# Performance work log

Measured on AMD Instinct MI355X. Metric: run time of the kernel, lower is better.

The kernel has to match this reference:

```python
import jax, jax.numpy as jnp
import numpy as np

N, E, LE, C = 20000, 320000, 640000, 128
EPS = 1e-7  # GENConv message eps


def _ln(x, g, b):
    # torch.nn.LayerNorm, eps=1e-5
    m = jnp.mean(x, axis=-1, keepdims=True)
    v = jnp.var(x, axis=-1, keepdims=True)
    return (x - m) * jax.lax.rsqrt(v + 1e-5) * g + b


def _mlp(x, W1, b1, g, b, W2, b2):
    # GENConv MLP, num_layers=2, norm='layer': Linear -> LayerNorm -> ReLU -> Linear
    h = jax.nn.relu(_ln(x @ W1 + b1, g, b))
    return h @ W2 + b2


def _gen_deep(x, src, dst, edge_attr, num_nodes, p):
    # DeepGCNLayer 'res+': norm -> relu -> dropout(eval=identity) -> GENConv -> + x
    h = jax.nn.relu(_ln(x, p['pre_g'], p['pre_b']))
    # GENConv message: relu(x_j [+ edge_attr]) + eps
    msg = h[src]
    if edge_attr is not None:
        msg = msg + edge_attr
    msg = jax.nn.relu(msg) + EPS  # [E, C]
    # softmax aggregation per destination segment, per channel
    logits = msg * p['t']
    mx = jax.ops.segment_max(logits, dst, num_segments=num_nodes)
    alpha = jnp.exp(logits - mx[dst])
    denom = jax.ops.segment_sum(alpha, dst, num_segments=num_nodes)
    aggr = jax.ops.segment_sum(alpha * msg, dst, num_segments=num_nodes)
    aggr = aggr / jnp.where(denom == 0, 1.0, denom)
    out = aggr + h  # GENConv root skip: out + x_r
    out = _mlp(out, p['W1'], p['b1'], p['ln_g'], p['ln_b'], p['W2'], p['b2'])
    return x + out  # res+ residual


def setup_inputs() -> dict:
    key = jax.random.key(0)
    ks = iter(jax.random.split(key, 16))
    s = 0.05
    d = {}
    d['v_x'] = jax.random.normal(next(ks), (N, C), jnp.float32)
    d['e_x'] = jax.random.normal(next(ks), (E, C), jnp.float32)
    d['v_edge_index'] = jax.random.randint(next(ks), (2, E), 0, N)
    d['e_edge_index'] = jax.random.randint(next(ks), (2, LE), 0, E)
    for pfx in ('e_', 'n_'):
        d[pfx + 'pre_g'] = jnp.ones((C,), jnp.float32)
        d[pfx + 'pre_b'] = jnp.zeros((C,), jnp.float32)
        d[pfx + 't'] = jnp.array(1.0, jnp.float32)
        d[pfx + 'W1'] = jax.random.normal(next(ks), (C, 2 * C), jnp.float32) * s
        d[pfx + 'b1'] = jnp.zeros((2 * C,), jnp.float32)
        d[pfx + 'ln_g'] = jnp.ones((2 * C,), jnp.float32)
        d[pfx + 'ln_b'] = jnp.zeros((2 * C,), jnp.float32)
        d[pfx + 'W2'] = jax.random.normal(next(ks), (2 * C, C), jnp.float32) * s
        d[pfx + 'b2'] = jnp.zeros((C,), jnp.float32)
    return d


def reference(v_x, e_x, v_edge_index, e_edge_index,
              e_pre_g, e_pre_b, e_t, e_W1, e_b1, e_ln_g, e_ln_b, e_W2, e_b2,
              n_pre_g, n_pre_b, n_t, n_W1, n_b1, n_ln_g, n_ln_b, n_W2, n_b2):
    ep = dict(pre_g=e_pre_g, pre_b=e_pre_b, t=e_t, W1=e_W1, b1=e_b1,
              ln_g=e_ln_g, ln_b=e_ln_b, W2=e_W2, b2=e_b2)
    npar = dict(pre_g=n_pre_g, pre_b=n_pre_b, t=n_t, W1=n_W1, b1=n_b1,
                ln_g=n_ln_g, ln_b=n_ln_b, W2=n_W2, b2=n_b2)
    # edge layer: GENConv over the line graph (no edge_attr)
    e_out = _gen_deep(e_x, e_edge_index[0], e_edge_index[1], None, E, ep)
    # node layer: GENConv over node graph with updated edge features as edge_attr
    v_out = _gen_deep(v_x, v_edge_index[0], v_edge_index[1], e_out, N, npar)
    return (v_out, e_out)
```

## Files before the change

kernel.cpp:

```cpp
#include <hip/hip_runtime.h>
#include <hip/hip_bf16.h>

#define GEN_EPS 1e-7f

typedef __attribute__((ext_vector_type(8))) short short8;
typedef __attribute__((ext_vector_type(4))) float f32x4;

__global__ void prep_all(
    const float* __restrict__ eW1, const float* __restrict__ eW2,
    const float* __restrict__ nW1, const float* __restrict__ nW2,
    short* __restrict__ eW1P, short* __restrict__ eW2P, short* __restrict__ nW1P,
    short* __restrict__ nW2P,
    const int* __restrict__ e_dst, const int* __restrict__ v_dst,
    int* __restrict__ ce, int* __restrict__ cn, int LE, int En, int nCNT,
    const float* __restrict__ ex, const float* __restrict__ vx,
    const float* __restrict__ eg, const float* __restrict__ eb,
    const float* __restrict__ ng, const float* __restrict__ nb_,
    __hip_bfloat16* __restrict__ he, __hip_bfloat16* __restrict__ hn, int E, int N) {
  int b = blockIdx.x;
  int tid = threadIdx.x;

  if (b < 768) {
    const float* W;
    short* WP;
    int R, Cc, c;
    if (b < 256) {
      W = eW1; WP = eW1P; R = 128; Cc = 256; c = b;
    } else if (b < 384) {
      W = eW2; WP = eW2P; R = 256; Cc = 128; c = b - 256;
    } else if (b < 640) {
      W = nW1; WP = nW1P; R = 128; Cc = 256; c = b - 384;
    } else {
      W = nW2; WP = nW2P; R = 256; Cc = 128; c = b - 640;
    }
    size_t tbase = (size_t)(c >> 4) * (size_t)(16 * R);
    int rsub = c & 15;
    for (int k = tid; k < R; k += blockDim.x) {
      __hip_bfloat16 bv = __float2bfloat16(W[(size_t)k * Cc + c]);
      int kk = k & 31;
      WP[tbase + (size_t)(k >> 5) * 512 + (kk >> 3) * 128 + rsub * 8 + (kk & 7)] =
          *(short*)&bv;
    }
    return;
  }
  b -= 768;

  if (b < nCNT) {
    int i = b * 256 + tid;
    if (i < LE)
      atomicAdd(&ce[e_dst[i]], 1);
    else if (i < LE + En)
      atomicAdd(&cn[v_dst[i - LE]], 1);
    return;
  }
  b -= nCNT;

  int l32 = tid & 31;
  int rr = b * 8 + ((tid & 255) >> 5);
  const float* x;
  const float* g;
  const float* bb;
  __hip_bfloat16* h;
  int r;
  if (rr < E) {
    x = ex; g = eg; bb = eb; h = he; r = rr;
  } else if (rr < E + N) {
    x = vx; g = ng; bb = nb_; h = hn; r = rr - E;
  } else {
    return;
  }
  float4 v = ((const float4*)(x + (size_t)r * 128))[l32];
  float s = v.x + v.y + v.z + v.w;
#pragma unroll
  for (int o = 16; o; o >>= 1) s += __shfl_xor(s, o);
  float m = s * (1.0f / 128.0f);
  float d0 = v.x - m, d1 = v.y - m, d2 = v.z - m, d3 = v.w - m;
  float q = d0 * d0 + d1 * d1 + d2 * d2 + d3 * d3;
#pragma unroll
  for (int o = 16; o; o >>= 1) q += __shfl_xor(q, o);
  float rstd = rsqrtf(q * (1.0f / 128.0f) + 1e-5f);
  float4 gv = ((const float4*)g)[l32];
  float4 bv = ((const float4*)bb)[l32];
  float2 h01, h23;
  h01.x = fmaxf(fmaf(d0 * rstd, gv.x, bv.x), 0.0f);
  h01.y = fmaxf(fmaf(d1 * rstd, gv.y, bv.y), 0.0f);
  h23.x = fmaxf(fmaf(d2 * rstd, gv.z, bv.z), 0.0f);
  h23.y = fmaxf(fmaf(d3 * rstd, gv.w, bv.w), 0.0f);
  __hip_bfloat162 p0 = __float22bfloat162_rn(h01);
  __hip_bfloat162 p1 = __float22bfloat162_rn(h23);
  uint2 u;
  u.x = *(uint*)&p0;
  u.y = *(uint*)&p1;
  ((uint2*)(h + (size_t)r * 128))[l32] = u;
}

__global__ void scan_block_sums_all(const int* __restrict__ ce, const int* __restrict__ cn,
                                    int* __restrict__ bsums, int nbE, int E, int N) {
  __shared__ int sm[256];
  int b = blockIdx.x;
  const int* counts;
  int M, bb;
  int* bs;
  if (b < nbE) {
    counts = ce; M = E; bb = b; bs = bsums;
  } else {
    counts = cn; M = N; bb = b - nbE; bs = bsums + 512;
  }
  int t = threadIdx.x;
  int base = bb * 1024 + t * 4;
  int s = 0;
#pragma unroll
  for (int i = 0; i < 4; i++) {
    int idx = base + i;
    if (idx < M) s += counts[idx];
  }
  sm[t] = s;
  __syncthreads();
  for (int o = 128; o; o >>= 1) {
    if (t < o) sm[t] += sm[t + o];
    __syncthreads();
  }
  if (t == 0) bs[bb] = sm[0];
}

__global__ void scan_bsums_all(int* bsums, int nbE, int nbN) {
  __shared__ int sm[512];
  int* bs = bsums + blockIdx.x * 512;
  int nb = (blockIdx.x == 0) ? nbE : nbN;
  int t = threadIdx.x;
  int v = (t < nb) ? bs[t] : 0;
  sm[t] = v;
  __syncthreads();
  for (int o = 1; o < 512; o <<= 1) {
    int u = (t >= o) ? sm[t - o] : 0;
    __syncthreads();
    sm[t] += u;
    __syncthreads();
  }
  if (t < nb) bs[t] = sm[t] - v;
}

__global__ void scan_write_all(const int* __restrict__ ce, const int* __restrict__ cn,
                               const int* __restrict__ bsums, int* __restrict__ off_e,
                               int* __restrict__ off_n, int* __restrict__ cur_e,
                               int* __restrict__ cur_n, int nbE, int E, int N, int LE,
                               int En) {
  __shared__ int sm[256];
  int b = blockIdx.x;
  const int* counts;
  const int* bs;
  int* off;
  int* cursor;
  int M, nnz, bb;
  if (b < nbE) {
    counts = ce; M = E; nnz = LE; bb = b; bs = bsums; off = off_e; cursor = cur_e;
  } else {
    counts = cn; M = N; nnz = En; bb = b - nbE; bs = bsums + 512; off = off_n;
    cursor = cur_n;
  }
  int t = threadIdx.x;
  int base = bb * 1024 + t * 4;
  int c[4];
  int s = 0;
#pragma unroll
  for (int i = 0; i < 4; i++) {
    int idx = base + i;
    c[i] = (idx < M) ? counts[idx] : 0;
    s += c[i];
  }
  sm[t] = s;
  __syncthreads();
  for (int o = 1; o < 256; o <<= 1) {
    int v = (t >= o) ? sm[t - o] : 0;
    __syncthreads();
    sm[t] += v;
    __syncthreads();
  }
  int p = bs[bb] + sm[t] - s;
#pragma unroll
  for (int i = 0; i < 4; i++) {
    int idx = base + i;
    if (idx < M) {
      off[idx] = p;
      cursor[idx] = p;
      p += c[i];
    }
  }
  if (bb == 0 && t == 0) off[M] = nnz;
}

__global__ void fill_all(const int* __restrict__ e_src, const int* __restrict__ e_dst,
                         const int* __restrict__ v_src, const int* __restrict__ v_dst,
                         int* __restrict__ cur_e, int* __restrict__ cur_n,
                         int* __restrict__ csrs_e, int* __restrict__ csrs_n,
                         int* __restrict__ csre_n, int LE, int En) {
  int i = blockIdx.x * blockDim.x + threadIdx.x;
  if (i < LE) {
    int p = atomicAdd(&cur_e[e_dst[i]], 1);
    csrs_e[p] = e_src[i];
  } else if (i < LE + En) {
    int j = i - LE;
    int p = atomicAdd(&cur_n[v_dst[j]], 1);
    csrs_n[p] = v_src[j];
    csre_n[p] = j;
  }
}

template <bool HAS_EATTR>
__global__ __launch_bounds__(256) void aggregate_kernel(
    const __hip_bfloat16* __restrict__ h, const int* __restrict__ off,
    const int* __restrict__ csr_src, const int* __restrict__ csr_eid,
    const ushort* __restrict__ eattr, const float* __restrict__ tptr,
    uint* __restrict__ yP, int M) {
  int lane = threadIdx.x & 63;
  int r = blockIdx.x * 4 + (threadIdx.x >> 6);
  if (r >= M) return;
  const float t = tptr[0];
  float2 hv = __bfloat1622float2(((const __hip_bfloat162*)(h + (size_t)r * 128))[lane]);
  int e0 = off[r], e1 = off[r + 1];
  float d0 = 0.0f, d1 = 0.0f, a0 = 0.0f, a1 = 0.0f;
  for (int e = e0; e < e1; e += 4) {
    int n = e1 - e;
    float2 mv[4];
#pragma unroll
    for (int u = 0; u < 4; u++) {
      int ee = (u < n) ? e + u : e;
      int s = csr_src[ee];
      mv[u] = __bfloat1622float2(((const __hip_bfloat162*)(h + (size_t)s * 128))[lane]);
    }
    if (HAS_EATTR) {
#pragma unroll
      for (int u = 0; u < 4; u++) {
        int ee = (u < n) ? e + u : e;
        int id = csr_eid[ee];
        uint ea = ((const uint*)(eattr + (size_t)id * 128))[lane];
        float2 ef = __bfloat1622float2(*(__hip_bfloat162*)&ea);
        mv[u].x += ef.x;
        mv[u].y += ef.y;
      }
    }
#pragma unroll
    for (int u = 0; u < 4; u++) {
      float w = (u < n) ? 1.0f : 0.0f;
      float m0 = fmaxf(mv[u].x, 0.0f) + GEN_EPS;
      float m1 = fmaxf(mv[u].y, 0.0f) + GEN_EPS;
      float al0 = __expf(m0 * t) * w, al1 = __expf(m1 * t) * w;
      d0 += al0;
      d1 += al1;
      a0 = fmaf(al0, m0, a0);
      a1 = fmaf(al1, m1, a1);
    }
  }
  float2 yv;
  yv.x = (e1 > e0 ? a0 / d0 : 0.0f) + hv.x;
  yv.y = (e1 > e0 ? a1 / d1 : 0.0f) + hv.y;
  __hip_bfloat162 yb2 = __float22bfloat162_rn(yv);
  yP[(r >> 4) * 1024 + (lane >> 4) * 256 + (r & 15) * 16 + (lane & 15)] = *(uint*)&yb2;
}

template <bool WRITE_BF16>
__global__ __launch_bounds__(512, 2) void mlp_kernel(
    const float* __restrict__ x, const short* yP, const short* __restrict__ W1P,
    const float* __restrict__ b1, const float* __restrict__ lng,
    const float* __restrict__ lnb, const short* __restrict__ W2P,
    const float* __restrict__ b2, float* __restrict__ out, ushort* out16,
    int ntiles, int stride, int M) {
  __shared__ short W1s[128 * 256];
  __shared__ short W2s[256 * 128];
  __shared__ short scr[8][2][16 * 34];

  const int tid = threadIdx.x, lane = tid & 63, wv = tid >> 6;
  const int rA = lane & 15, hi = lane >> 4;
  const int kA = hi * 8, jrow = hi * 4;
  const int foW = lane * 8;
  const int foA = rA * 32 + kA;

  {
    const short8* g1 = (const short8*)W1P;
    short8* l1 = (short8*)W1s;
#pragma unroll
    for (int i = 0; i < 8; i++) l1[i * 512 + tid] = g1[i * 512 + tid];
    const short8* g2 = (const short8*)W2P;
    short8* l2 = (short8*)W2s;
#pragma unroll
    for (int i = 0; i < 8; i++) l2[i * 512 + tid] = g2[i * 512 + tid];
  }

  float b1v[16], lngv[16], lnbv[16], b2v[8];
#pragma unroll
  for (int ct = 0; ct < 16; ct++) {
    int col = ct * 16 + rA;
    b1v[ct] = b1[col];
    lngv[ct] = lng[col];
    lnbv[ct] = lnb[col];
  }
#pragma unroll
  for (int ct = 0; ct < 8; ct++) b2v[ct] = b2[ct * 16 + rA];

  __syncthreads();

  int t = blockIdx.x * 8 + wv;
  short8 yA0, yA1, yA2, yA3;
  if (t < ntiles) {
    const short* yb = yP + (size_t)t * 2048 + foA;
    yA0 = *(const short8*)(yb);
    yA1 = *(const short8*)(yb + 512);
    yA2 = *(const short8*)(yb + 1024);
    yA3 = *(const short8*)(yb + 1536);
  }

  for (; t < ntiles; t += stride) {
    const int row0 = t * 16;

    f32x4 C1[16];
#pragma unroll
    for (int i = 0; i < 16; i++) C1[i] = (f32x4)0.0f;
#pragma unroll
    for (int kc = 0; kc < 4; kc++) {
      short8 a = (kc == 0) ? yA0 : (kc == 1) ? yA1 : (kc == 2) ? yA2 : yA3;
#pragma unroll
      for (int ct = 0; ct < 16; ct++) {
        short8 B = *(const short8*)&W1s[(ct * 4 + kc) * 512 + foW];
        C1[ct] = __builtin_amdgcn_mfma_f32_16x16x32_bf16(a, B, C1[ct], 0, 0, 0);
      }
    }

    {
      int tn = t + stride;
      int tc = (tn < ntiles) ? tn : t;
      const short* yb = yP + (size_t)tc * 2048 + foA;
      yA0 = *(const short8*)(yb);
      yA1 = *(const short8*)(yb + 512);
      yA2 = *(const short8*)(yb + 1024);
      yA3 = *(const short8*)(yb + 1536);
    }

    float xv[32];
#pragma unroll
    for (int ct = 0; ct < 8; ct++)
#pragma unroll
      for (int j = 0; j < 4; j++) {
        int row = row0 + jrow + j;
        int rr = (row < M) ? row : (M - 1);
        xv[ct * 4 + j] = x[(size_t)rr * 128 + ct * 16 + rA];
      }

#pragma unroll
    for (int ct = 0; ct < 16; ct++)
#pragma unroll
      for (int j = 0; j < 4; j++) C1[ct][j] += b1v[ct];

    float mean[4], rstd[4];
#pragma unroll
    for (int j = 0; j < 4; j++) {
      float p = 0.0f, q = 0.0f;
#pragma unroll
      for (int ct = 0; ct < 16; ct++) {
        p += C1[ct][j];
        q = fmaf(C1[ct][j], C1[ct][j], q);
      }
#pragma unroll
      for (int o = 1; o < 16; o <<= 1) {
        p += __shfl_xor(p, o);
        q += __shfl_xor(q, o);
      }
      float m = p * (1.0f / 256.0f);
      mean[j] = m;
      rstd[j] = rsqrtf(q * (1.0f / 256.0f) - m * m + 1e-5f);
    }

    f32x4 C2[8];
#pragma unroll
    for (int i = 0; i < 8; i++) C2[i] = (f32x4)0.0f;
#pragma unroll
    for (int kc = 0; kc < 8; kc++) {
      short* s = &scr[wv][kc & 1][0];
#pragma unroll
      for (int ct2 = 0; ct2 < 2; ct2++) {
        int ctg = kc * 2 + ct2;
#pragma unroll
        for (int j = 0; j < 4; j++) {
          float v =
              fmaxf(fmaf((C1[ctg][j] - mean[j]) * rstd[j], lngv[ctg], lnbv[ctg]), 0.0f);
          __hip_bfloat16 bv = __float2bfloat16(v);
          s[(jrow + j) * 34 + ct2 * 16 + rA] = *(short*)&bv;
        }
      }
      asm volatile("s_waitcnt lgkmcnt(0)" ::: "memory");
      __builtin_amdgcn_sched_barrier(0);
      short8 a = *(const short8*)&s[rA * 34 + kA];
#pragma unroll
      for (int ct = 0; ct < 8; ct++) {
        short8 B = *(const short8*)&W2s[(ct * 8 + kc) * 512 + foW];
        C2[ct] = __builtin_amdgcn_mfma_f32_16x16x32_bf16(a, B, C2[ct], 0, 0, 0);
      }
    }

#pragma unroll
    for (int ct = 0; ct < 8; ct++) {
#pragma unroll
      for (int j = 0; j < 4; j++) {
        int row = row0 + jrow + j;
        if (row < M) {
          size_t idx = (size_t)row * 128 + ct * 16 + rA;
          float o = C2[ct][j] + b2v[ct] + xv[ct * 4 + j];
          out[idx] = o;
          if (WRITE_BF16) {
            __hip_bfloat16 bo = __float2bfloat16(o);
            out16[idx] = *(ushort*)&bo;
          }
        }
      }
    }
  }
}

extern "C" void kernel_launch(void* const* d_in, const int* in_sizes, int n_in,
                              void* d_out, int out_size, void* d_ws, size_t ws_size,
                              hipStream_t stream) {
  const int C = 128;
  const float* v_x = (const float*)d_in[0];
  const float* e_x = (const float*)d_in[1];
  const int* v_ei = (const int*)d_in[2];
  const int* e_ei = (const int*)d_in[3];
  const int N = in_sizes[0] / C;
  const int E = in_sizes[1] / C;
  const int LE = in_sizes[3] / 2;

  const float* ep[9];
  const float* np_[9];
  for (int i = 0; i < 9; i++) ep[i] = (const float*)d_in[4 + i];
  for (int i = 0; i < 9; i++) np_[i] = (const float*)d_in[13 + i];

  float* v_out = (float*)d_out;
  float* e_out = (float*)d_out + (size_t)N * C;

  char* wsp = (char*)d_ws;
  size_t o = 0;
  auto carve = [&](size_t bytes) {
    void* p = wsp + o;
    o += (bytes + 255) & ~(size_t)255;
    return p;
  };
  short* yPe = (short*)carve((size_t)E * C * 2);
  short* yPn = (short*)carve((size_t)N * C * 2);
  int* counts = (int*)carve((size_t)(E + N) * 4);
  int* off_e = (int*)carve(((size_t)E + 1) * 4);
  int* off_n = (int*)carve(((size_t)N + 1) * 4);
  int* cur_e = (int*)carve((size_t)E * 4);
  int* cur_n = (int*)carve((size_t)N * 4);
  int* bsums = (int*)carve(4096);
  int* csrs_e = (int*)carve((size_t)LE * 4);
  int* csrs_n = (int*)carve((size_t)E * 4);
  int* csre_n = (int*)carve((size_t)E * 4);
  short* eW1P = (short*)carve((size_t)256 * 128 * 2);
  short* eW2P = (short*)carve((size_t)128 * 256 * 2);
  short* nW1P = (short*)carve((size_t)256 * 128 * 2);
  short* nW2P = (short*)carve((size_t)128 * 256 * 2);
  (void)ws_size;
  (void)n_in;
  (void)out_size;

  int* counts_e = counts;
  int* counts_n = counts + E;
  __hip_bfloat16* h_e = (__hip_bfloat16*)e_out;
  __hip_bfloat16* h_n = (__hip_bfloat16*)v_out;

  hipMemsetAsync(counts, 0, (size_t)(E + N) * 4, stream);
  int nCNT = (LE + E + 255) / 256;
  int nLN = (E + N + 7) / 8;
  prep_all<<<768 + nCNT + nLN, 256, 0, stream>>>(
      ep[3], ep[7], np_[3], np_[7], eW1P, eW2P, nW1P, nW2P, e_ei + LE, v_ei + E,
      counts_e, counts_n, LE, E, nCNT, e_x, v_x, ep[0], ep[1], np_[0], np_[1], h_e, h_n,
      E, N);
  int nbE = (E + 1023) / 1024, nbN = (N + 1023) / 1024;
  scan_block_sums_all<<<nbE + nbN, 256, 0, stream>>>(counts_e, counts_n, bsums, nbE, E, N);
  scan_bsums_all<<<2, 512, 0, stream>>>(bsums, nbE, nbN);
  scan_write_all<<<nbE + nbN, 256, 0, stream>>>(counts_e, counts_n, bsums, off_e, off_n,
                                                cur_e, cur_n, nbE, E, N, LE, E);
  fill_all<<<(LE + E + 255) / 256, 256, 0, stream>>>(e_ei, e_ei + LE, v_ei, v_ei + E,
                                                     cur_e, cur_n, csrs_e, csrs_n, csre_n,
                                                     LE, E);

  aggregate_kernel<false><<<(E + 3) / 4, 256, 0, stream>>>(h_e, off_e, csrs_e, nullptr,
                                                           nullptr, ep[2], (uint*)yPe, E);
  {
    int ntiles = (E + 15) / 16;
    int gblocks = (ntiles + 7) / 8;
    if (gblocks > 256) gblocks = 256;
    int stride = gblocks * 8;
    mlp_kernel<true><<<gblocks, 512, 0, stream>>>(e_x, yPe, eW1P, ep[4], ep[5], ep[6],
                                                  eW2P, ep[8], e_out, (ushort*)yPe,
                                                  ntiles, stride, E);
  }

  aggregate_kernel<true><<<(N + 3) / 4, 256, 0, stream>>>(h_n, off_n, csrs_n, csre_n,
                                                          (const ushort*)yPe, np_[2],
                                                          (uint*)yPn, N);
  {
    int ntiles = (N + 15) / 16;
    int gblocks = (ntiles + 7) / 8;
    if (gblocks > 256) gblocks = 256;
    int stride = gblocks * 8;
    mlp_kernel<false><<<gblocks, 512, 0, stream>>>(v_x, yPn, nW1P, np_[4], np_[5], np_[6],
                                                   nW2P, np_[8], v_out, nullptr, ntiles,
                                                   stride, N);
  }
}
```

Before: 404.6 us.

## Fuse three-pass CSR offset scan into single-pass decoupled look-back scan

Replaces the three scan kernels (block sums, scan of block sums, write) with one kernel that uses a decoupled look-back: each block publishes its aggregate and inclusive prefix as flagged 64-bit values and spins on its predecessors. The edge-count atomics move out of prep_all into a separate count_all kernel, which also zeroes the flag array. This removes two kernel launches and a pass over the counts. In exchange, correctness depends on blocks being scheduled in order, since a block spins on earlier blocks, and the look-back walk is serial.

New measurement: 410.9 us. About the same (+1.6%).

```diff
diff --git a/kernel.cpp b/kernel.cpp
--- a/kernel.cpp
+++ b/kernel.cpp
@@ -5,14 +5,25 @@
 
 typedef __attribute__((ext_vector_type(8))) short short8;
 typedef __attribute__((ext_vector_type(4))) float f32x4;
+
+__global__ void count_all(const int* __restrict__ e_dst, const int* __restrict__ v_dst,
+                          int* __restrict__ ce, int* __restrict__ cn,
+                          unsigned long long* __restrict__ part, int LE, int En) {
+  if (blockIdx.x == 0) {
+    for (int k = threadIdx.x; k < 1024; k += 256) part[k] = 0ULL;
+  }
+  int i = blockIdx.x * 256 + threadIdx.x;
+  if (i < LE)
+    atomicAdd(&ce[e_dst[i]], 1);
+  else if (i < LE + En)
+    atomicAdd(&cn[v_dst[i - LE]], 1);
+}
 
 __global__ void prep_all(
     const float* __restrict__ eW1, const float* __restrict__ eW2,
     const float* __restrict__ nW1, const float* __restrict__ nW2,
     short* __restrict__ eW1P, short* __restrict__ eW2P, short* __restrict__ nW1P,
     short* __restrict__ nW2P,
-    const int* __restrict__ e_dst, const int* __restrict__ v_dst,
-    int* __restrict__ ce, int* __restrict__ cn, int LE, int En, int nCNT,
     const float* __restrict__ ex, const float* __restrict__ vx,
     const float* __restrict__ eg, const float* __restrict__ eb,
     const float* __restrict__ ng, const float* __restrict__ nb_,
@@ -44,16 +55,6 @@
     return;
   }
   b -= 768;
-
-  if (b < nCNT) {
-    int i = b * 256 + tid;
-    if (i < LE)
-      atomicAdd(&ce[e_dst[i]], 1);
-    else if (i < LE + En)
-      atomicAdd(&cn[v_dst[i - LE]], 1);
-    return;
-  }
-  b -= nCNT;
 
   int l32 = tid & 31;
   int rr = b * 8 + ((tid & 255) >> 5);
@@ -94,69 +95,24 @@
   ((uint2*)(h + (size_t)r * 128))[l32] = u;
 }
 
-__global__ void scan_block_sums_all(const int* __restrict__ ce, const int* __restrict__ cn,
-                                    int* __restrict__ bsums, int nbE, int E, int N) {
+__global__ void scan_fused(const int* __restrict__ ce, const int* __restrict__ cn,
+                           unsigned long long* __restrict__ part,
+                           int* __restrict__ off_e, int* __restrict__ off_n,
+                           int* __restrict__ cur_e, int* __restrict__ cur_n,
+                           int nbE, int E, int N, int LE, int En) {
   __shared__ int sm[256];
+  __shared__ int smPrev;
   int b = blockIdx.x;
   const int* counts;
-  int M, bb;
-  int* bs;
-  if (b < nbE) {
-    counts = ce; M = E; bb = b; bs = bsums;
-  } else {
-    counts = cn; M = N; bb = b - nbE; bs = bsums + 512;
-  }
-  int t = threadIdx.x;
-  int base = bb * 1024 + t * 4;
-  int s = 0;
-#pragma unroll
-  for (int i = 0; i < 4; i++) {
-    int idx = base + i;
-    if (idx < M) s += counts[idx];
-  }
-  sm[t] = s;
-  __syncthreads();
-  for (int o = 128; o; o >>= 1) {
-    if (t < o) sm[t] += sm[t + o];
-    __syncthreads();
-  }
-  if (t == 0) bs[bb] = sm[0];
-}
-
-__global__ void scan_bsums_all(int* bsums, int nbE, int nbN) {
-  __shared__ int sm[512];
-  int* bs = bsums + blockIdx.x * 512;
-  int nb = (blockIdx.x == 0) ? nbE : nbN;
-  int t = threadIdx.x;
-  int v = (t < nb) ? bs[t] : 0;
-  sm[t] = v;
-  __syncthreads();
-  for (int o = 1; o < 512; o <<= 1) {
-    int u = (t >= o) ? sm[t - o] : 0;
-    __syncthreads();
-    sm[t] += u;
-    __syncthreads();
-  }
-  if (t < nb) bs[t] = sm[t] - v;
-}
-
-__global__ void scan_write_all(const int* __restrict__ ce, const int* __restrict__ cn,
-                               const int* __restrict__ bsums, int* __restrict__ off_e,
-                               int* __restrict__ off_n, int* __restrict__ cur_e,
-                               int* __restrict__ cur_n, int nbE, int E, int N, int LE,
-                               int En) {
-  __shared__ int sm[256];
-  int b = blockIdx.x;
-  const int* counts;
-  const int* bs;
+  int M, nnz, bb;
   int* off;
   int* cursor;
-  int M, nnz, bb;
+  unsigned long long* pr;
   if (b < nbE) {
-    counts = ce; M = E; nnz = LE; bb = b; bs = bsums; off = off_e; cursor = cur_e;
+    counts = ce; M = E; nnz = LE; bb = b; off = off_e; cursor = cur_e; pr = part;
   } else {
-    counts = cn; M = N; nnz = En; bb = b - nbE; bs = bsums + 512; off = off_n;
-    cursor = cur_n;
+    counts = cn; M = N; nnz = En; bb = b - nbE; off = off_n; cursor = cur_n;
+    pr = part + 512;
   }
   int t = threadIdx.x;
   int base = bb * 1024 + t * 4;
@@ -176,7 +132,29 @@
     sm[t] += v;
     __syncthreads();
   }
-  int p = bs[bb] + sm[t] - s;
+  int total = sm[255];
+  if (t == 0) {
+    int prev = 0;
+    if (bb == 0) {
+      atomicExch(&pr[0], (2ULL << 32) | (unsigned long long)(unsigned)total);
+    } else {
+      atomicExch(&pr[bb], (1ULL << 32) | (unsigned long long)(unsigned)total);
+      int j = bb - 1;
+      while (true) {
+        unsigned long long v;
+        do {
+          v = atomicAdd(&pr[j], 0ULL);
+        } while ((v >> 32) == 0ULL);
+        prev += (int)(v & 0xffffffffULL);
+        if ((v >> 32) == 2ULL) break;
+        j--;
+      }
+      atomicExch(&pr[bb], (2ULL << 32) | (unsigned long long)(unsigned)(prev + total));
+    }
+    smPrev = prev;
+  }
+  __syncthreads();
+  int p = smPrev + sm[t] - s;
 #pragma unroll
   for (int i = 0; i < 4; i++) {
     int idx = base + i;
@@ -449,7 +427,7 @@
   int* off_n = (int*)carve(((size_t)N + 1) * 4);
   int* cur_e = (int*)carve((size_t)E * 4);
   int* cur_n = (int*)carve((size_t)N * 4);
-  int* bsums = (int*)carve(4096);
+  unsigned long long* part = (unsigned long long*)carve(1024 * 8);
   int* csrs_e = (int*)carve((size_t)LE * 4);
   int* csrs_n = (int*)carve((size_t)E * 4);
   int* csre_n = (int*)carve((size_t)E * 4);
@@ -467,17 +445,15 @@
   __hip_bfloat16* h_n = (__hip_bfloat16*)v_out;
 
   hipMemsetAsync(counts, 0, (size_t)(E + N) * 4, stream);
-  int nCNT = (LE + E + 255) / 256;
+  count_all<<<(LE + E + 255) / 256, 256, 0, stream>>>(e_ei + LE, v_ei + E, counts_e,
+                                                      counts_n, part, LE, E);
   int nLN = (E + N + 7) / 8;
-  prep_all<<<768 + nCNT + nLN, 256, 0, stream>>>(
-      ep[3], ep[7], np_[3], np_[7], eW1P, eW2P, nW1P, nW2P, e_ei + LE, v_ei + E,
-      counts_e, counts_n, LE, E, nCNT, e_x, v_x, ep[0], ep[1], np_[0], np_[1], h_e, h_n,
-      E, N);
+  prep_all<<<768 + nLN, 256, 0, stream>>>(ep[3], ep[7], np_[3], np_[7], eW1P, eW2P,
+                                          nW1P, nW2P, e_x, v_x, ep[0], ep[1], np_[0],
+                                          np_[1], h_e, h_n, E, N);
   int nbE = (E + 1023) / 1024, nbN = (N + 1023) / 1024;
-  scan_block_sums_all<<<nbE + nbN, 256, 0, stream>>>(counts_e, counts_n, bsums, nbE, E, N);
-  scan_bsums_all<<<2, 512, 0, stream>>>(bsums, nbE, nbN);
-  scan_write_all<<<nbE + nbN, 256, 0, stream>>>(counts_e, counts_n, bsums, off_e, off_n,
-                                                cur_e, cur_n, nbE, E, N, LE, E);
+  scan_fused<<<nbE + nbN, 256, 0, stream>>>(counts_e, counts_n, part, off_e, off_n,
+                                            cur_e, cur_n, nbE, E, N, LE, E);
   fill_all<<<(LE + E + 255) / 256, 256, 0, stream>>>(e_ei, e_ei + LE, v_ei, v_ei + E,
                                                      cur_e, cur_n, csrs_e, csrs_n, csre_n,
                                                      LE, E);
```
